# Kernel tuning notes

Hardware: AMD Instinct MI355X
Metric: run time of the kernel (lower is better)

Reference implementation:

```python
import jax, jax.numpy as jnp
import numpy as np

N_EMBD = 1024
N_HEAD = 16
HEAD_DIM = N_EMBD // N_HEAD


def setup_inputs() -> dict:
    key = jax.random.key(0)
    kx, kq, kk, kv, ko = jax.random.split(key, 5)
    s = 1.0 / np.sqrt(N_EMBD)
    return {
        "x": jax.random.normal(kx, (4, 2048, N_EMBD), dtype=jnp.float32),
        "Wq": jax.random.normal(kq, (N_EMBD, N_EMBD), dtype=jnp.float32) * s,
        "Wk": jax.random.normal(kk, (N_EMBD, N_EMBD), dtype=jnp.float32) * s,
        "Wv": jax.random.normal(kv, (N_EMBD, N_EMBD), dtype=jnp.float32) * s,
        "Wo": jax.random.normal(ko, (N_EMBD, N_EMBD), dtype=jnp.float32) * s,
    }


def reference(x, Wq, Wk, Wv, Wo):
    B, T, C = x.shape
    H, D = N_HEAD, HEAD_DIM
    # projections; torch Linear computes x @ W.T
    q = (x @ Wq.T).reshape(B, T, H, D).transpose(0, 2, 1, 3)  # [B,H,T,D]
    k = (x @ Wk.T).reshape(B, T, H, D).transpose(0, 2, 1, 3)
    v = (x @ Wv.T).reshape(B, T, H, D).transpose(0, 2, 1, 3)
    scores = jnp.einsum("bhtd,bhsd->bhts", q, k) / np.sqrt(D).astype(np.float32)
    causal = jnp.tril(jnp.ones((T, T), dtype=bool))
    scores = jnp.where(causal, scores, -jnp.inf)
    attn = jax.nn.softmax(scores, axis=-1)
    out = jnp.einsum("bhts,bhsd->bhtd", attn, v)  # [B,H,T,D]
    out = out.transpose(0, 2, 1, 3).reshape(B, T, C)
    return out @ Wo.T
```

## Files before the change

### kernel.cpp

```cpp
#include <hip/hip_runtime.h>
#include <hip/hip_bf16.h>


typedef __bf16 bf16_t;
typedef __bf16 bf16x4 __attribute__((ext_vector_type(4)));
typedef __bf16 bf16x8 __attribute__((ext_vector_type(8)));
typedef float  f32x4  __attribute__((ext_vector_type(4)));

#define MFMA16(a, b, c) __builtin_amdgcn_mfma_f32_16x16x32_bf16(a, b, c, 0, 0, 0)

__device__ __forceinline__ float exp2_(float x) {
#if __has_builtin(__builtin_amdgcn_exp2f)
    return __builtin_amdgcn_exp2f(x);
#else
    return __expf(x * 0.6931471805599453f);
#endif
}

__device__ __forceinline__ void gload_lds16(const bf16_t* g, bf16_t* l) {
    __builtin_amdgcn_global_load_lds(
        (const __attribute__((address_space(1))) void*)g,
        (__attribute__((address_space(3))) void*)l, 16, 0, 0);
}

__global__ __launch_bounds__(256)
void cast_all(const float* __restrict__ x,  const float* __restrict__ Wq,
              const float* __restrict__ Wk, const float* __restrict__ Wv,
              const float* __restrict__ Wo,
              bf16_t* __restrict__ xb, bf16_t* __restrict__ wqkv,
              bf16_t* __restrict__ wob) {
    int i = blockIdx.x * 256 + threadIdx.x;
    const float* src;
    bf16_t* dst;
    if (blockIdx.y == 0) {
        src = x; dst = xb;
    } else {
        if (i >= 524288) return;
        int wsel = i >> 17;
        int loc  = i & 131071;
        src = wsel == 0 ? Wq : wsel == 1 ? Wk : wsel == 2 ? Wv : Wo;
        dst = wsel == 3 ? wob : wqkv + (size_t)wsel * 1048576;
        i = loc;
    }
    const float4* p = (const float4*)src;
    float4 a = p[i * 2], b = p[i * 2 + 1];
    bf16x8 o;
    o[0] = (bf16_t)a.x; o[1] = (bf16_t)a.y; o[2] = (bf16_t)a.z; o[3] = (bf16_t)a.w;
    o[4] = (bf16_t)b.x; o[5] = (bf16_t)b.y; o[6] = (bf16_t)b.z; o[7] = (bf16_t)b.w;
    *(bf16x8*)(dst + (size_t)i * 8) = o;
}

template<int OUT_BF16>
__global__ __launch_bounds__(256)
void gemm_bt(const bf16_t* __restrict__ A, const bf16_t* __restrict__ B,
             void* __restrict__ Cv, int M, int N, int K) {
    __shared__ bf16_t As[128 * 32];
    __shared__ bf16_t Bs[128 * 32];
    const int tid = threadIdx.x;
    const int lane = tid & 63;
    const int w = tid >> 6;
    const int wm = w >> 1, wn = w & 1;
    const int g = lane >> 4, c = lane & 15;
    const long bm = (long)blockIdx.x * 128;
    const long bn = (long)blockIdx.y * 128;

    f32x4 acc[4][4] = {};

    const int srow = tid >> 2;
    const int scol = (tid & 3) << 3;
    const bf16_t* Ag = A + (bm + srow) * (long)K + scol;
    const bf16_t* Bg = B + (bn + srow) * (long)K + scol;
    bf16_t* AsW = As + tid * 8;
    bf16_t* BsW = Bs + tid * 8;

    for (int k0 = 0; k0 < K; k0 += 32) {
        gload_lds16(Ag + k0,                 AsW);
        gload_lds16(Ag + k0 + (long)64 * K,  AsW + 2048);
        gload_lds16(Bg + k0,                 BsW);
        gload_lds16(Bg + k0 + (long)64 * K,  BsW + 2048);
        __syncthreads();
        bf16x8 af[4], bfr[4];
        #pragma unroll
        for (int m = 0; m < 4; ++m)
            af[m] = *(const bf16x8*)(As + (wm * 64 + m * 16 + c) * 32 + g * 8);
        #pragma unroll
        for (int n = 0; n < 4; ++n)
            bfr[n] = *(const bf16x8*)(Bs + (wn * 64 + n * 16 + c) * 32 + g * 8);
        #pragma unroll
        for (int m = 0; m < 4; ++m)
            #pragma unroll
            for (int n = 0; n < 4; ++n)
                acc[m][n] = MFMA16(af[m], bfr[n], acc[m][n]);
        __syncthreads();
    }
    #pragma unroll
    for (int m = 0; m < 4; ++m)
        #pragma unroll
        for (int n = 0; n < 4; ++n)
            #pragma unroll
            for (int i = 0; i < 4; ++i) {
                long row = bm + wm * 64 + m * 16 + g * 4 + i;
                long col = bn + wn * 64 + n * 16 + c;
                float v = acc[m][n][i];
                if (OUT_BF16) ((bf16_t*)Cv)[row * N + col] = (bf16_t)v;
                else          ((float*)Cv)[row * N + col]  = v;
            }
}


__device__ __forceinline__ void stage_K(const bf16_t* Kp, long rowb, int kb, int hcol,
                                        bf16_t* Kbuf, int tid) {
    int row = tid >> 3;
    int lb  = (tid & 7) ^ (row & 7);
    gload_lds16(Kp + (rowb + kb + row) * 3072 + hcol + lb * 8, Kbuf + tid * 8);
}

__device__ __forceinline__ bf16x8 load_V8(const bf16_t* Vp, long rowb, int kb,
                                          int hcol, int tid) {
    const int d  = tid & 63;
    const int k0 = (tid >> 6) * 8;
    bf16x8 v;
    #pragma unroll
    for (int j = 0; j < 8; ++j)
        v[j] = Vp[(rowb + kb + k0 + j) * 3072 + hcol + d];
    return v;
}

__device__ __forceinline__ void write_V8(bf16_t* Vbuf, int tid, bf16x8 v) {
    const int d  = tid & 63;
    const int k0 = (tid >> 6) * 8;
    *(bf16x8*)&Vbuf[d * 72 + k0] = v;
}

__global__ __launch_bounds__(512, 6)
void attn_kernel(const bf16_t* __restrict__ Qp, const bf16_t* __restrict__ Kp,
                 const bf16_t* __restrict__ Vp, bf16_t* __restrict__ O) {
    __shared__ bf16_t Ks[2][64 * 64];
    __shared__ bf16_t Vts[2][64 * 72];
    __shared__ bf16_t PW[8][16 * 72];

    const int tid = threadIdx.x, lane = tid & 63, w = tid >> 6;
    const int g = lane >> 4, c = lane & 15;
    const int bh = blockIdx.x;
    const int b = bh >> 4, h = bh & 15;
    const long rowb = (long)b * 2048;
    const int hcol = h * 64;
    const float QSCL = 0.18033688011112042f;

    const int q0  = 15 - blockIdx.y;
    const int qlo = q0 * 128 + w * 16;
    const int nkt = 2 * q0 + 2;

    bf16x8 qf[2];
    #pragma unroll
    for (int ks = 0; ks < 2; ++ks) {
        qf[ks] = *(const bf16x8*)(Qp + (rowb + qlo + c) * 3072 +
                                  hcol + ks * 32 + g * 8);
        #pragma unroll
        for (int j = 0; j < 8; ++j)
            qf[ks][j] = (bf16_t)((float)qf[ks][j] * QSCL);
    }

    float m_r = -1e30f;
    float l_r = 0.f;
    f32x4 acc[4] = {};

    stage_K(Kp, rowb, 0, hcol, Ks[0], tid);
    write_V8(Vts[0], tid, load_V8(Vp, rowb, 0, hcol, tid));
    __syncthreads();

    for (int t = 0; t < nkt; ++t) {
        const int cur = t & 1;
        const int kb = t * 64;
        const bool pre = (t + 1 < nkt);
        bf16x8 vreg;
        if (pre) {
            stage_K(Kp, rowb, kb + 64, hcol, Ks[cur ^ 1], tid);
            vreg = load_V8(Vp, rowb, kb + 64, hcol, tid);
        }

        if (kb <= qlo + 15) {
            f32x4 sacc[4] = {};
            __builtin_amdgcn_s_setprio(1);
            #pragma unroll
            for (int nt = 0; nt < 4; ++nt) {
                const int row = nt * 16 + c;
                #pragma unroll
                for (int ks = 0; ks < 2; ++ks) {
                    bf16x8 kf = *(const bf16x8*)&Ks[cur][row * 64 +
                                    (((ks * 4 + g) ^ (c & 7)) * 8)];
                    sacc[nt] = MFMA16(kf, qf[ks], sacc[nt]);
                }
            }
            __builtin_amdgcn_s_setprio(0);
            if (kb + 63 > qlo) {
                const int q = qlo + c;
                #pragma unroll
                for (int nt = 0; nt < 4; ++nt)
                    #pragma unroll
                    for (int i = 0; i < 4; ++i) {
                        int key = kb + nt * 16 + g * 4 + i;
                        if (key > q) sacc[nt][i] = -1e30f;
                    }
            }

            float m0 = fmaxf(fmaxf(sacc[0][0], sacc[0][1]),
                             fmaxf(fmaxf(sacc[0][2], sacc[0][3]), sacc[1][0]));
            float m1 = fmaxf(fmaxf(sacc[1][1], sacc[1][2]),
                             fmaxf(fmaxf(sacc[1][3], sacc[2][0]), sacc[2][1]));
            float m2 = fmaxf(fmaxf(sacc[2][2], sacc[2][3]),
                             fmaxf(fmaxf(sacc[3][0], sacc[3][1]),
                                   fmaxf(sacc[3][2], sacc[3][3])));
            float mx = fmaxf(fmaxf(m0, m1), m2);
            if (__any(mx > m_r + 8.f)) {
                mx = fmaxf(mx, __shfl_xor(mx, 16, 64));
                mx = fmaxf(mx, __shfl_xor(mx, 32, 64));
                float mnew = fmaxf(m_r, mx);
                float scl = exp2_(m_r - mnew);
                #pragma unroll
                for (int nt = 0; nt < 4; ++nt)
                    acc[nt] *= scl;
                l_r *= scl;
                m_r = mnew;
            }
            float rsn[4];
            #pragma unroll
            for (int nt = 0; nt < 4; ++nt) {
                #pragma unroll
                for (int i = 0; i < 4; ++i)
                    sacc[nt][i] = exp2_(sacc[nt][i] - m_r);
                rsn[nt] = (sacc[nt][0] + sacc[nt][1]) + (sacc[nt][2] + sacc[nt][3]);
            }
            l_r += (rsn[0] + rsn[1]) + (rsn[2] + rsn[3]);

            #pragma unroll
            for (int nt = 0; nt < 4; ++nt) {
                bf16x4 t4;
                #pragma unroll
                for (int i = 0; i < 4; ++i) t4[i] = (bf16_t)sacc[nt][i];
                *(bf16x4*)&PW[w][c * 72 + nt * 16 + g * 4] = t4;
            }

            __builtin_amdgcn_s_setprio(1);
            #pragma unroll
            for (int ks = 0; ks < 2; ++ks) {
                bf16x8 pf = *(const bf16x8*)&PW[w][c * 72 + ks * 32 + g * 8];
                #pragma unroll
                for (int nt = 0; nt < 4; ++nt) {
                    bf16x8 vf = *(const bf16x8*)&Vts[cur][(nt * 16 + c) * 72 +
                                                          ks * 32 + g * 8];
                    acc[nt] = MFMA16(vf, pf, acc[nt]);
                }
            }
            __builtin_amdgcn_s_setprio(0);
        }

        if (pre) write_V8(Vts[cur ^ 1], tid, vreg);
        __syncthreads();
    }

    l_r += __shfl_xor(l_r, 16, 64);
    l_r += __shfl_xor(l_r, 32, 64);
    {
        float rl = __builtin_amdgcn_rcpf(l_r);
        #pragma unroll
        for (int nt = 0; nt < 4; ++nt) {
            bf16x4 t4;
            #pragma unroll
            for (int i = 0; i < 4; ++i) t4[i] = (bf16_t)(acc[nt][i] * rl);
            *(bf16x4*)&PW[w][c * 72 + nt * 16 + g * 4] = t4;
        }
    }
    #pragma unroll
    for (int p = 0; p < 2; ++p) {
        int row = p * 8 + (lane >> 3);
        int ch  = (lane & 7) * 8;
        bf16x8 v = *(const bf16x8*)&PW[w][row * 72 + ch];
        *(bf16x8*)&O[(rowb + qlo + row) * 1024 + hcol + ch] = v;
    }
}

extern "C" void kernel_launch(void* const* d_in, const int* in_sizes, int n_in,
                              void* d_out, int out_size, void* d_ws, size_t ws_size,
                              hipStream_t stream) {
    const float* x  = (const float*)d_in[0];
    const float* Wq = (const float*)d_in[1];
    const float* Wk = (const float*)d_in[2];
    const float* Wv = (const float*)d_in[3];
    const float* Wo = (const float*)d_in[4];

    const int M = 8192;
    const int C = 1024;

    char* ws = (char*)d_ws;
    bf16_t* xb   = (bf16_t*)(ws);
    bf16_t* wqkv = (bf16_t*)(ws + ((size_t)16 << 20));
    bf16_t* wob  = (bf16_t*)(ws + ((size_t)22 << 20));
    bf16_t* qkv  = (bf16_t*)(ws + ((size_t)24 << 20));
    bf16_t* aob  = (bf16_t*)(ws + ((size_t)72 << 20));

    cast_all<<<dim3(4096, 2), 256, 0, stream>>>(x, Wq, Wk, Wv, Wo, xb, wqkv, wob);

    gemm_bt<1><<<dim3(M / 128, 3072 / 128), 256, 0, stream>>>(xb, wqkv, qkv, M, 3072, C);

    attn_kernel<<<dim3(64, 16), 512, 0, stream>>>(
        qkv, qkv + 1024, qkv + 2048, aob);

    gemm_bt<0><<<dim3(M / 128, C / 128), 256, 0, stream>>>(aob, wob, d_out, M, C, C);
}
```

Baseline: 179.7 us.

## Replace GEMM with 256x128 tile, 8-wave double-buffered phased pipeline

Replaces the simple single-buffered GEMM with a 512-thread kernel using 256x128 tiles, K-step 64, XOR-swizzled LDS layout and double buffering. Global-to-LDS loads for the next tile are issued inside per-row MFMA phases, gated by explicit waitcnt, barriers and setprio. The aim is to hide memory latency, avoid LDS bank conflicts and raise MFMA utilisation in both projection GEMMs. In exchange the kernel uses 96KB of LDS per block and relies on hand-placed synchronisation that is fragile to get right.

```diff
diff --git a/kernel.cpp b/kernel.cpp
--- a/kernel.cpp
+++ b/kernel.cpp
@@ -51,56 +51,106 @@
 }
 
 template<int OUT_BF16>
-__global__ __launch_bounds__(256)
-void gemm_bt(const bf16_t* __restrict__ A, const bf16_t* __restrict__ B,
-             void* __restrict__ Cv, int M, int N, int K) {
-    __shared__ bf16_t As[128 * 32];
-    __shared__ bf16_t Bs[128 * 32];
+__global__ __launch_bounds__(512, 2)
+void gemm_8ph(const bf16_t* __restrict__ A, const bf16_t* __restrict__ B,
+              void* __restrict__ Cv, int M, int N, int K) {
+    __shared__ bf16_t sm[2][24576];
     const int tid = threadIdx.x;
-    const int lane = tid & 63;
-    const int w = tid >> 6;
-    const int wm = w >> 1, wn = w & 1;
+    const int lane = tid & 63, w = tid >> 6;
+    const int wr = w >> 1, wc = w & 1;
     const int g = lane >> 4, c = lane & 15;
-    const long bm = (long)blockIdx.x * 128;
+    const long bm = (long)blockIdx.x * 256;
     const long bn = (long)blockIdx.y * 128;
 
+    const int srow8 = tid >> 3;
+    const int pb = tid & 7;
+
+    auto STAGE_A = [&](int buf, int h, int kt) {
+        #pragma unroll
+        for (int r = 0; r < 2; ++r) {
+            int row = h * 128 + r * 64 + srow8;
+            int lb  = pb ^ (row & 7);
+            gload_lds16(A + (bm + row) * (long)K + kt * 64 + lb * 8,
+                        &sm[buf][row * 64 + pb * 8]);
+        }
+    };
+    auto STAGE_B = [&](int buf, int kt) {
+        #pragma unroll
+        for (int r = 0; r < 2; ++r) {
+            int row = r * 64 + srow8;
+            int lb  = pb ^ (row & 7);
+            gload_lds16(B + (bn + row) * (long)K + kt * 64 + lb * 8,
+                        &sm[buf][16384 + row * 64 + pb * 8]);
+        }
+    };
+    auto LDA = [&](int buf, int m, int k) -> bf16x8 {
+        int row = wr * 64 + m * 16 + c;
+        return *(const bf16x8*)&sm[buf][row * 64 + (((k * 4 + g) ^ (row & 7)) * 8)];
+    };
+    auto LDB = [&](int buf, int n, int k) -> bf16x8 {
+        int row = wc * 64 + n * 16 + c;
+        return *(const bf16x8*)&sm[buf][16384 + row * 64 +
+                                        (((k * 4 + g) ^ (row & 7)) * 8)];
+    };
+
+#define PHASE(BUF, MM, ISSUE_STMT, WAIT_STMT)                          \
+    {                                                                  \
+        bf16x8 a0 = LDA(BUF, MM, 0), a1 = LDA(BUF, MM, 1);             \
+        ISSUE_STMT;                                                    \
+        WAIT_STMT;                                                     \
+        __builtin_amdgcn_s_barrier();                                  \
+        asm volatile("s_waitcnt lgkmcnt(0)" ::: "memory");             \
+        __builtin_amdgcn_sched_barrier(0);                             \
+        __builtin_amdgcn_s_setprio(1);                                 \
+        _Pragma("unroll")                                              \
+        for (int n = 0; n < 4; ++n) {                                  \
+            acc[MM][n] = MFMA16(a0, bfr[n][0], acc[MM][n]);            \
+            acc[MM][n] = MFMA16(a1, bfr[n][1], acc[MM][n]);            \
+        }                                                              \
+        __builtin_amdgcn_s_setprio(0);                                 \
+        __builtin_amdgcn_s_barrier();                                  \
+    }
+
     f32x4 acc[4][4] = {};
-
-    const int srow = tid >> 2;
-    const int scol = (tid & 3) << 3;
-    const bf16_t* Ag = A + (bm + srow) * (long)K + scol;
-    const bf16_t* Bg = B + (bn + srow) * (long)K + scol;
-    bf16_t* AsW = As + tid * 8;
-    bf16_t* BsW = Bs + tid * 8;
-
-    for (int k0 = 0; k0 < K; k0 += 32) {
-        gload_lds16(Ag + k0,                 AsW);
-        gload_lds16(Ag + k0 + (long)64 * K,  AsW + 2048);
-        gload_lds16(Bg + k0,                 BsW);
-        gload_lds16(Bg + k0 + (long)64 * K,  BsW + 2048);
-        __syncthreads();
-        bf16x8 af[4], bfr[4];
-        #pragma unroll
-        for (int m = 0; m < 4; ++m)
-            af[m] = *(const bf16x8*)(As + (wm * 64 + m * 16 + c) * 32 + g * 8);
-        #pragma unroll
-        for (int n = 0; n < 4; ++n)
-            bfr[n] = *(const bf16x8*)(Bs + (wn * 64 + n * 16 + c) * 32 + g * 8);
-        #pragma unroll
-        for (int m = 0; m < 4; ++m)
-            #pragma unroll
-            for (int n = 0; n < 4; ++n)
-                acc[m][n] = MFMA16(af[m], bfr[n], acc[m][n]);
-        __syncthreads();
-    }
+    bf16x8 bfr[4][2];
+    const int NJ = K / 128;
+
+    STAGE_B(0, 0); STAGE_A(0, 0, 0); STAGE_A(0, 1, 0);
+    STAGE_B(1, 1);
+    asm volatile("s_waitcnt vmcnt(2)" ::: "memory");
+    __builtin_amdgcn_s_barrier();
+
+    for (int j = 0; j < NJ; ++j) {
+        const int t0 = 2 * j;
+        const bool more = (j + 1 < NJ);
+
+        #pragma unroll
+        for (int n = 0; n < 4; ++n) { bfr[n][0] = LDB(0, n, 0); bfr[n][1] = LDB(0, n, 1); }
+        PHASE(0, 0, STAGE_A(1, 0, t0 + 1), (void)0);
+        PHASE(0, 1, STAGE_A(1, 1, t0 + 1), (void)0);
+        PHASE(0, 2, if (more) STAGE_B(0, t0 + 2), (void)0);
+        PHASE(0, 3, (void)0,
+              if (more) { asm volatile("s_waitcnt vmcnt(2)" ::: "memory"); }
+              else      { asm volatile("s_waitcnt vmcnt(0)" ::: "memory"); });
+
+        #pragma unroll
+        for (int n = 0; n < 4; ++n) { bfr[n][0] = LDB(1, n, 0); bfr[n][1] = LDB(1, n, 1); }
+        PHASE(1, 0, if (more) STAGE_A(0, 0, t0 + 2), (void)0);
+        PHASE(1, 1, if (more) STAGE_A(0, 1, t0 + 2), (void)0);
+        PHASE(1, 2, if (more) STAGE_B(1, t0 + 3), (void)0);
+        PHASE(1, 3, (void)0,
+              if (more) { asm volatile("s_waitcnt vmcnt(2)" ::: "memory"); });
+    }
+#undef PHASE
+
     #pragma unroll
     for (int m = 0; m < 4; ++m)
         #pragma unroll
         for (int n = 0; n < 4; ++n)
             #pragma unroll
             for (int i = 0; i < 4; ++i) {
-                long row = bm + wm * 64 + m * 16 + g * 4 + i;
-                long col = bn + wn * 64 + n * 16 + c;
+                long row = bm + wr * 64 + m * 16 + g * 4 + i;
+                long col = bn + wc * 64 + n * 16 + c;
                 float v = acc[m][n][i];
                 if (OUT_BF16) ((bf16_t*)Cv)[row * N + col] = (bf16_t)v;
                 else          ((float*)Cv)[row * N + col]  = v;
@@ -301,10 +351,10 @@
 
     cast_all<<<dim3(4096, 2), 256, 0, stream>>>(x, Wq, Wk, Wv, Wo, xb, wqkv, wob);
 
-    gemm_bt<1><<<dim3(M / 128, 3072 / 128), 256, 0, stream>>>(xb, wqkv, qkv, M, 3072, C);
+    gemm_8ph<1><<<dim3(M / 256, 3072 / 128), 512, 0, stream>>>(xb, wqkv, qkv, M, 3072, C);
 
     attn_kernel<<<dim3(64, 16), 512, 0, stream>>>(
         qkv, qkv + 1024, qkv + 2048, aob);
 
-    gemm_bt<0><<<dim3(M / 128, C / 128), 256, 0, stream>>>(aob, wob, d_out, M, C, C);
-}
+    gemm_8ph<0><<<dim3(M / 256, C / 128), 512, 0, stream>>>(aob, wob, d_out, M, C, C);
+}
```

Result: faster. 159.8 us (median of 2 runs) (-11.0%).
